# Performance work log

Measured on AMD Instinct MI355X. Metric: run time of the kernel, lower is better.

Reference implementation:

```python
import jax, jax.numpy as jnp
import numpy as np

N_NODES = 100000
N_EDGES = 1600000
D_FEAT = 128
D_OUT = 128


def gcn_conv(x, W, b, src, dst, w, n):
    # symmetric normalization (PyG GCNConv with self-loops already appended)
    deg = jax.ops.segment_sum(w, dst, num_segments=n)
    dinv = jnp.where(deg > 0, jax.lax.rsqrt(deg), 0.0)
    norm = dinv[src] * w * dinv[dst]                       # [E]
    h = x @ W                                              # [N, Dout]
    out = jax.ops.segment_sum(h[src] * norm[:, None], dst, num_segments=n)
    return out + b


def setup_inputs() -> dict:
    key = jax.random.key(0)
    ks = jax.random.split(key, 20)
    feat = jax.random.normal(ks[0], (N_NODES, D_FEAT), dtype=jnp.float32)
    gdv = jax.random.uniform(ks[1], (N_NODES, 73), dtype=jnp.float32)
    pr = jax.random.uniform(ks[2], (N_NODES, 1), dtype=jnp.float32)
    edge_index = jax.random.randint(ks[3], (2, N_EDGES), 0, N_NODES, dtype=jnp.int32)
    edge_weight = jax.random.uniform(ks[4], (N_EDGES,), dtype=jnp.float32)

    def lin(k, fi, fo):
        bound = 1.0 / np.sqrt(fi)
        k1, k2 = jax.random.split(k)
        W = jax.random.uniform(k1, (fi, fo), minval=-bound, maxval=bound, dtype=jnp.float32)
        b = jax.random.uniform(k2, (fo,), minval=-bound, maxval=bound, dtype=jnp.float32)
        return W, b

    W1, b1 = lin(ks[5], D_FEAT, D_OUT)          # gcn_layer1
    W2, b2 = lin(ks[6], D_OUT, D_OUT // 2)      # gcn_layer2
    gdv_W, gdv_b = lin(ks[7], 73, D_OUT // 4)
    pr_W, pr_b = lin(ks[8], 1, D_OUT // 4)
    enc_W1, enc_b1 = lin(ks[9], D_OUT, D_OUT)
    enc_W2, enc_b2 = lin(ks[10], D_OUT, D_OUT)
    return dict(feat=feat, gdv=gdv, pr=pr, edge_index=edge_index, edge_weight=edge_weight,
                W1=W1, b1=b1, W2=W2, b2=b2, gdv_W=gdv_W, gdv_b=gdv_b, pr_W=pr_W, pr_b=pr_b,
                enc_W1=enc_W1, enc_b1=enc_b1, enc_W2=enc_W2, enc_b2=enc_b2)


def reference(feat, gdv, pr, edge_index, edge_weight,
              W1, b1, W2, b2, gdv_W, gdv_b, pr_W, pr_b,
              enc_W1, enc_b1, enc_W2, enc_b2):
    n = feat.shape[0]
    loop = jnp.arange(n, dtype=edge_index.dtype)
    src = jnp.concatenate([edge_index[0], loop])
    dst = jnp.concatenate([edge_index[1], loop])
    w = jnp.concatenate([edge_weight, jnp.ones((n,), dtype=edge_weight.dtype)])

    h = jnp.tanh(gcn_conv(feat, W1, b1, src, dst, w, n))
    adj = jax.nn.sigmoid(gcn_conv(h, W2, b2, src, dst, w, n))   # [N, D/2]

    g = jax.nn.sigmoid(gdv @ gdv_W + gdv_b)                      # [N, D/4]
    p = jax.nn.sigmoid(pr @ pr_W + pr_b)                         # [N, D/4]

    enc = jnp.concatenate([adj, g, p], axis=1)                   # [N, D]
    enc = jnp.tanh(enc @ enc_W1 + enc_b1) @ enc_W2 + enc_b2
    return enc
```

## Files before the change

kernel.cpp:

```cpp
#include <hip/hip_runtime.h>
#include <hip/hip_bf16.h>
#include <cstdint>
#include <cstddef>

#define TPB 256
#define SCAN_CHUNK 1024

typedef short bf16x8 __attribute__((ext_vector_type(8)));
typedef float f32x4 __attribute__((ext_vector_type(4)));

__device__ __forceinline__ float sigmoidf_(float x) {
    return 1.0f / (1.0f + __expf(-x));
}
__device__ __forceinline__ unsigned short f2bf(float x) {
    unsigned u = __float_as_uint(x);
    u += 0x7FFF + ((u >> 16) & 1);
    return (unsigned short)(u >> 16);
}
__device__ __forceinline__ float bf2f(unsigned short b) {
    return __uint_as_float(((unsigned)b) << 16);
}

__device__ __forceinline__ void gld_lds16(const void* gsrc, void* ldst) {
    __builtin_amdgcn_global_load_lds(
        (const __attribute__((address_space(1))) unsigned*)gsrc,
        (__attribute__((address_space(3))) unsigned*)ldst, 16, 0, 0);
}

template<int M>
__device__ __forceinline__ void prep_w_body(const float* __restrict__ W,
                                            unsigned short* __restrict__ Wt, int c) {
    if (c >= M * 16) return;
    int m = c >> 4, k0 = (c & 15) << 3;
    unsigned o[4];
    #pragma unroll
    for (int j = 0; j < 4; ++j) {
        unsigned lo = f2bf(W[(size_t)(k0 + 2 * j) * M + m]);
        unsigned hi = f2bf(W[(size_t)(k0 + 2 * j + 1) * M + m]);
        o[j] = lo | (hi << 16);
    }
    unsigned byte = ((unsigned)c * 16) ^ (unsigned)((m & 7) << 4);
    *(uint4*)((char*)Wt + byte) = *(uint4*)o;
}

__global__ __launch_bounds__(TPB) void k_prep(const float* W1, unsigned short* wt1,
                                              const float* W2, unsigned short* wt2,
                                              const float* E1, unsigned short* wtE1,
                                              const float* E2, unsigned short* wtE2,
                                              unsigned* counts, int n, int nbZ) {
    int bid = blockIdx.x;
    if (bid < nbZ) {
        int i = bid * TPB + threadIdx.x;
        if (i < n) counts[i] = 0u;
    } else {
        int t = bid - nbZ;
        if (t < 8)       prep_w_body<128>(W1, wt1, t * TPB + threadIdx.x);
        else if (t < 12) prep_w_body<64>(W2, wt2, (t - 8) * TPB + threadIdx.x);
        else if (t < 20) prep_w_body<128>(E1, wtE1, (t - 12) * TPB + threadIdx.x);
        else             prep_w_body<128>(E2, wtE2, (t - 20) * TPB + threadIdx.x);
    }
}

template<int M, int ACT, bool A_BF16, bool OUT_F32>
__device__ __forceinline__ void mgemm_body(const void* __restrict__ Ap,
                                           const unsigned short* __restrict__ Wtg,
                                           const float* __restrict__ bias,
                                           void* __restrict__ Cp, int ldc, int coff,
                                           int n, int tile,
                                           unsigned short* Al, unsigned short* Wt) {
    const int tid = threadIdx.x;
    const int wv = tid >> 6;
    const int ln = tid & 63;
    const int rbase = tile * 128;

    constexpr int WCH = (M * 128 * 2) / 1024;
    #pragma unroll
    for (int c = 0; c < WCH / 4; ++c) {
        int cc = wv * (WCH / 4) + c;
        gld_lds16((const char*)Wtg + cc * 1024 + ln * 16, (char*)Wt + cc * 1024);
    }

    if (A_BF16 && rbase + 128 <= n) {
        #pragma unroll
        for (int it = 0; it < 8; ++it) {
            unsigned dbase = (unsigned)(wv * 8 + it) * 1024;
            unsigned d = dbase + (unsigned)ln * 16;
            unsigned row = d >> 8;
            unsigned s = d ^ ((row & 7) << 4);
            gld_lds16((const char*)Ap + (size_t)rbase * 256 + s, (char*)Al + dbase);
        }
    } else {
        for (int ch = tid; ch < 128 * 16; ch += TPB) {
            int row = ch >> 4;
            int col8 = (ch & 15) * 8;
            int r = rbase + row;
            unsigned o4[4] = {0u, 0u, 0u, 0u};
            if (r < n) {
                if constexpr (A_BF16) {
                    uint4 v = *(const uint4*)((const unsigned short*)Ap + (size_t)r * 128 + col8);
                    o4[0] = v.x; o4[1] = v.y; o4[2] = v.z; o4[3] = v.w;
                } else {
                    float4 a = *(const float4*)((const float*)Ap + (size_t)r * 128 + col8);
                    float4 b = *(const float4*)((const float*)Ap + (size_t)r * 128 + col8 + 4);
                    o4[0] = (unsigned)f2bf(a.x) | ((unsigned)f2bf(a.y) << 16);
                    o4[1] = (unsigned)f2bf(a.z) | ((unsigned)f2bf(a.w) << 16);
                    o4[2] = (unsigned)f2bf(b.x) | ((unsigned)f2bf(b.y) << 16);
                    o4[3] = (unsigned)f2bf(b.z) | ((unsigned)f2bf(b.w) << 16);
                }
            }
            unsigned byte = ((unsigned)ch * 16) ^ (unsigned)((row & 7) << 4);
            *(uint4*)((char*)Al + byte) = *(uint4*)o4;
        }
    }
    __syncthreads();

    const int lr = ln & 15;
    const int lg = ln >> 4;

    constexpr int MF = M / 16;
    f32x4 acc[2][MF];
    #pragma unroll
    for (int i = 0; i < 2; ++i)
        #pragma unroll
        for (int j = 0; j < MF; ++j) acc[i][j] = (f32x4){0.f, 0.f, 0.f, 0.f};

    #pragma unroll
    for (int kk = 0; kk < 4; ++kk) {
        const int kb = kk * 64 + lg * 16;
        bf16x8 af[2];
        #pragma unroll
        for (int rf = 0; rf < 2; ++rf) {
            int row = wv * 32 + rf * 16 + lr;
            unsigned byte = (unsigned)(row * 256 + kb) ^ (unsigned)((row & 7) << 4);
            af[rf] = *(bf16x8*)((char*)Al + byte);
        }
        #pragma unroll
        for (int mf = 0; mf < MF; ++mf) {
            int col = mf * 16 + lr;
            unsigned byte = (unsigned)(col * 256 + kb) ^ (unsigned)((col & 7) << 4);
            bf16x8 bfg = *(bf16x8*)((char*)Wt + byte);
            acc[0][mf] = __builtin_amdgcn_mfma_f32_16x16x32_bf16(af[0], bfg, acc[0][mf], 0, 0, 0);
            acc[1][mf] = __builtin_amdgcn_mfma_f32_16x16x32_bf16(af[1], bfg, acc[1][mf], 0, 0, 0);
        }
    }

    #pragma unroll
    for (int rf = 0; rf < 2; ++rf) {
        #pragma unroll
        for (int j = 0; j < 4; ++j) {
            int row = rbase + wv * 32 + rf * 16 + lg * 4 + j;
            if (row < n) {
                #pragma unroll
                for (int mf = 0; mf < MF; ++mf) {
                    int col = mf * 16 + lr;
                    float v = acc[rf][mf][j] + (bias ? bias[col] : 0.0f);
                    if constexpr (ACT == 1) v = tanhf(v);
                    else if constexpr (ACT == 2) v = sigmoidf_(v);
                    if constexpr (OUT_F32)
                        ((float*)Cp)[(size_t)row * ldc + coff + col] = v;
                    else
                        ((unsigned short*)Cp)[(size_t)row * ldc + coff + col] = f2bf(v);
                }
            }
        }
    }
}

__global__ __launch_bounds__(TPB) void k_g1p1(const float* __restrict__ feat,
                                              const unsigned short* __restrict__ wt1,
                                              unsigned short* __restrict__ bufA,
                                              int n, int nbM,
                                              const int* __restrict__ dst,
                                              unsigned* __restrict__ counts,
                                              unsigned* __restrict__ epos, int E) {
    __shared__ __align__(16) unsigned short Al[128 * 128];
    __shared__ __align__(16) unsigned short Wt[128 * 128];
    if (blockIdx.x < nbM) {
        mgemm_body<128, 0, false, false>(feat, wt1, nullptr, bufA, 128, 0, n,
                                         blockIdx.x, Al, Wt);
    } else {
        int e = (blockIdx.x - nbM) * TPB + threadIdx.x;
        if (e < E) epos[e] = atomicAdd(&counts[dst[e]], 1u);
    }
}

__global__ __launch_bounds__(TPB) void k_mgemm64(const unsigned short* __restrict__ Ap,
                                                 const unsigned short* __restrict__ Wtg,
                                                 unsigned short* __restrict__ Cp, int n) {
    __shared__ __align__(16) unsigned short Al[128 * 128];
    __shared__ __align__(16) unsigned short Wt[64 * 128];
    mgemm_body<64, 0, true, false>(Ap, Wtg, nullptr, Cp, 64, 0, n, blockIdx.x, Al, Wt);
}

__global__ __launch_bounds__(TPB) void k_enc2(const unsigned short* __restrict__ enc,
                                              const unsigned short* __restrict__ w1g,
                                              const float* __restrict__ b1,
                                              const unsigned short* __restrict__ w2g,
                                              const float* __restrict__ b2,
                                              float* __restrict__ out, int n) {
    __shared__ __align__(16) unsigned short Al[128 * 128];
    __shared__ __align__(16) unsigned short Wt[128 * 128];
    const int tid = threadIdx.x;
    const int wv = tid >> 6;
    const int ln = tid & 63;
    const int rbase = blockIdx.x * 128;
    const int lr = ln & 15;
    const int lg = ln >> 4;

    #pragma unroll
    for (int c = 0; c < 8; ++c) {
        int cc = wv * 8 + c;
        gld_lds16((const char*)w1g + cc * 1024 + ln * 16, (char*)Wt + cc * 1024);
    }
    if (rbase + 128 <= n) {
        #pragma unroll
        for (int it = 0; it < 8; ++it) {
            unsigned dbase = (unsigned)(wv * 8 + it) * 1024;
            unsigned d = dbase + (unsigned)ln * 16;
            unsigned row = d >> 8;
            unsigned s = d ^ ((row & 7) << 4);
            gld_lds16((const char*)enc + (size_t)rbase * 256 + s, (char*)Al + dbase);
        }
    } else {
        for (int ch = tid; ch < 128 * 16; ch += TPB) {
            int row = ch >> 4;
            int col8 = (ch & 15) * 8;
            int r = rbase + row;
            unsigned o4[4] = {0u, 0u, 0u, 0u};
            if (r < n) {
                uint4 v = *(const uint4*)(enc + (size_t)r * 128 + col8);
                o4[0] = v.x; o4[1] = v.y; o4[2] = v.z; o4[3] = v.w;
            }
            unsigned byte = ((unsigned)ch * 16) ^ (unsigned)((row & 7) << 4);
            *(uint4*)((char*)Al + byte) = *(uint4*)o4;
        }
    }
    __syncthreads();

    f32x4 acc[2][8];
    #pragma unroll
    for (int i = 0; i < 2; ++i)
        #pragma unroll
        for (int j = 0; j < 8; ++j) acc[i][j] = (f32x4){0.f, 0.f, 0.f, 0.f};

    #pragma unroll
    for (int kk = 0; kk < 4; ++kk) {
        const int kb = kk * 64 + lg * 16;
        bf16x8 af[2];
        #pragma unroll
        for (int rf = 0; rf < 2; ++rf) {
            int row = wv * 32 + rf * 16 + lr;
            unsigned byte = (unsigned)(row * 256 + kb) ^ (unsigned)((row & 7) << 4);
            af[rf] = *(bf16x8*)((char*)Al + byte);
        }
        #pragma unroll
        for (int mf = 0; mf < 8; ++mf) {
            int col = mf * 16 + lr;
            unsigned byte = (unsigned)(col * 256 + kb) ^ (unsigned)((col & 7) << 4);
            bf16x8 bfg = *(bf16x8*)((char*)Wt + byte);
            acc[0][mf] = __builtin_amdgcn_mfma_f32_16x16x32_bf16(af[0], bfg, acc[0][mf], 0, 0, 0);
            acc[1][mf] = __builtin_amdgcn_mfma_f32_16x16x32_bf16(af[1], bfg, acc[1][mf], 0, 0, 0);
        }
    }
    __syncthreads();

    #pragma unroll
    for (int c = 0; c < 8; ++c) {
        int cc = wv * 8 + c;
        gld_lds16((const char*)w2g + cc * 1024 + ln * 16, (char*)Wt + cc * 1024);
    }
    #pragma unroll
    for (int rf = 0; rf < 2; ++rf) {
        #pragma unroll
        for (int j = 0; j < 4; ++j) {
            int rl = wv * 32 + rf * 16 + lg * 4 + j;
            #pragma unroll
            for (int mf = 0; mf < 8; ++mf) {
                int col = mf * 16 + lr;
                float v = tanhf(acc[rf][mf][j] + b1[col]);
                unsigned byte = (unsigned)(rl * 256 + col * 2) ^ (unsigned)((rl & 7) << 4);
                *(unsigned short*)((char*)Al + byte) = f2bf(v);
            }
        }
    }
    __syncthreads();

    #pragma unroll
    for (int i = 0; i < 2; ++i)
        #pragma unroll
        for (int j = 0; j < 8; ++j) acc[i][j] = (f32x4){0.f, 0.f, 0.f, 0.f};

    #pragma unroll
    for (int kk = 0; kk < 4; ++kk) {
        const int kb = kk * 64 + lg * 16;
        bf16x8 af[2];
        #pragma unroll
        for (int rf = 0; rf < 2; ++rf) {
            int row = wv * 32 + rf * 16 + lr;
            unsigned byte = (unsigned)(row * 256 + kb) ^ (unsigned)((row & 7) << 4);
            af[rf] = *(bf16x8*)((char*)Al + byte);
        }
        #pragma unroll
        for (int mf = 0; mf < 8; ++mf) {
            int col = mf * 16 + lr;
            unsigned byte = (unsigned)(col * 256 + kb) ^ (unsigned)((col & 7) << 4);
            bf16x8 bfg = *(bf16x8*)((char*)Wt + byte);
            acc[0][mf] = __builtin_amdgcn_mfma_f32_16x16x32_bf16(af[0], bfg, acc[0][mf], 0, 0, 0);
            acc[1][mf] = __builtin_amdgcn_mfma_f32_16x16x32_bf16(af[1], bfg, acc[1][mf], 0, 0, 0);
        }
    }

    #pragma unroll
    for (int rf = 0; rf < 2; ++rf) {
        #pragma unroll
        for (int j = 0; j < 4; ++j) {
            int row = rbase + wv * 32 + rf * 16 + lg * 4 + j;
            if (row < n) {
                #pragma unroll
                for (int mf = 0; mf < 8; ++mf) {
                    int col = mf * 16 + lr;
                    out[(size_t)row * 128 + col] = acc[rf][mf][j] + b2[col];
                }
            }
        }
    }
}


__global__ __launch_bounds__(TPB) void k_scan_a(const unsigned* __restrict__ counts,
                                                int* __restrict__ rowptr,
                                                int* __restrict__ bsums, int n) {
    __shared__ int s[SCAN_CHUNK];
    int base = blockIdx.x * SCAN_CHUNK;
    int orig[4];
    #pragma unroll
    for (int j0 = 0; j0 < 4; ++j0) {
        int j = threadIdx.x + j0 * TPB;
        int v = (base + j < n) ? (int)counts[base + j] : 0;
        orig[j0] = v;
        s[j] = v;
    }
    __syncthreads();
    for (int off = 1; off < SCAN_CHUNK; off <<= 1) {
        int t[4];
        #pragma unroll
        for (int j0 = 0; j0 < 4; ++j0) {
            int j = threadIdx.x + j0 * TPB;
            t[j0] = (j >= off) ? s[j - off] : 0;
        }
        __syncthreads();
        #pragma unroll
        for (int j0 = 0; j0 < 4; ++j0) {
            int j = threadIdx.x + j0 * TPB;
            s[j] += t[j0];
        }
        __syncthreads();
    }
    #pragma unroll
    for (int j0 = 0; j0 < 4; ++j0) {
        int j = threadIdx.x + j0 * TPB;
        if (base + j < n) rowptr[base + j] = s[j] - orig[j0];
    }
    if (threadIdx.x == 0) bsums[blockIdx.x] = s[SCAN_CHUNK - 1];
}

__global__ void k_scan_b(int* bsums, int nb) {
    __shared__ int s[128];
    int t = threadIdx.x;
    int v = (t < nb) ? bsums[t] : 0;
    s[t] = v;
    __syncthreads();
    for (int off = 1; off < 128; off <<= 1) {
        int x = (t >= off) ? s[t - off] : 0;
        __syncthreads();
        s[t] += x;
        __syncthreads();
    }
    if (t < nb) bsums[t] = s[t] - v;
}

__global__ __launch_bounds__(TPB) void k_scan_c(int* __restrict__ rowptr,
                                                const int* __restrict__ bsums,
                                                int n, int E) {
    int i = blockIdx.x * TPB + threadIdx.x;
    if (i < n) rowptr[i] += bsums[i / SCAN_CHUNK];
    if (i == 0) rowptr[n] = E;
}

__global__ __launch_bounds__(TPB) void k_fill(const int* __restrict__ src,
                                              const int* __restrict__ dst,
                                              const float* __restrict__ ew,
                                              const int* __restrict__ rowptr,
                                              const unsigned* __restrict__ epos,
                                              uint2* __restrict__ edges, int E) {
    int e = blockIdx.x * TPB + threadIdx.x;
    if (e < E) {
        unsigned slot = (unsigned)rowptr[dst[e]] + epos[e];
        uint2 pk;
        pk.x = (unsigned)src[e];
        pk.y = __float_as_uint(ew[e]);
        edges[slot] = pk;
    }
}

__global__ __launch_bounds__(TPB) void k_deg(const int* __restrict__ rowptr,
                                             const uint2* __restrict__ edges,
                                             float* __restrict__ dinv, int n) {
    int i = blockIdx.x * TPB + threadIdx.x;
    if (i >= n) return;
    int beg = rowptr[i], end = rowptr[i + 1];
    float s = 1.0f;
    for (int e = beg; e < end; ++e) s += __uint_as_float(edges[e].y);
    dinv[i] = rsqrtf(s);
}

template<int D, int ACT>
__device__ __forceinline__ void agg_body(const unsigned short* __restrict__ h,
                                         const int* __restrict__ rowptr,
                                         const uint2* __restrict__ edges,
                                         const float* __restrict__ dinv,
                                         const float* __restrict__ bias,
                                         unsigned short* __restrict__ out,
                                         int ldo, int n, int node) {
    const int lane = threadIdx.x & 63;
    constexpr int PER = D / 64;
    float acc[PER];
    const float di = dinv[node];
    if constexpr (PER == 2) {
        unsigned hv = *(const unsigned*)&h[(size_t)node * D + lane * 2];
        acc[0] = bf2f((unsigned short)hv) * di;
        acc[1] = bf2f((unsigned short)(hv >> 16)) * di;
    } else {
        acc[0] = bf2f(h[(size_t)node * D + lane]) * di;
    }
    const int beg = rowptr[node];
    const int end = rowptr[node + 1];
    for (int e = beg; e < end; e += 8) {
        int ss[8]; float ww[8];
        #pragma unroll
        for (int u = 0; u < 8; ++u) {
            int idx = e + u;
            int cl = idx < end ? idx : (end - 1);
            uint2 ed = edges[cl];
            ss[u] = (int)ed.x;
            ww[u] = idx < end ? __uint_as_float(ed.y) : 0.0f;
        }
        float nn[8];
        #pragma unroll
        for (int u = 0; u < 8; ++u) nn[u] = ww[u] * dinv[ss[u]];
        if constexpr (PER == 2) {
            unsigned hv[8];
            #pragma unroll
            for (int u = 0; u < 8; ++u)
                hv[u] = *(const unsigned*)&h[(size_t)ss[u] * D + lane * 2];
            #pragma unroll
            for (int u = 0; u < 8; ++u) {
                acc[0] += bf2f((unsigned short)hv[u]) * nn[u];
                acc[1] += bf2f((unsigned short)(hv[u] >> 16)) * nn[u];
            }
        } else {
            unsigned short hv[8];
            #pragma unroll
            for (int u = 0; u < 8; ++u) hv[u] = h[(size_t)ss[u] * D + lane];
            #pragma unroll
            for (int u = 0; u < 8; ++u) acc[0] += bf2f(hv[u]) * nn[u];
        }
    }
    if constexpr (PER == 2) {
        float v0 = acc[0] * di + bias[lane * 2];
        float v1 = acc[1] * di + bias[lane * 2 + 1];
        if constexpr (ACT == 1) { v0 = tanhf(v0); v1 = tanhf(v1); }
        else                    { v0 = sigmoidf_(v0); v1 = sigmoidf_(v1); }
        unsigned pk = (unsigned)f2bf(v0) | ((unsigned)f2bf(v1) << 16);
        *(unsigned*)&out[(size_t)node * ldo + lane * 2] = pk;
    } else {
        float v = acc[0] * di + bias[lane];
        v = (ACT == 1) ? tanhf(v) : sigmoidf_(v);
        out[(size_t)node * ldo + lane] = f2bf(v);
    }
}

__global__ __launch_bounds__(TPB) void k_agg128(const unsigned short* __restrict__ h,
                                                const int* __restrict__ rowptr,
                                                const uint2* __restrict__ edges,
                                                const float* __restrict__ dinv,
                                                const float* __restrict__ bias,
                                                unsigned short* __restrict__ out, int n) {
    int node = blockIdx.x * 4 + (threadIdx.x >> 6);
    if (node < n) agg_body<128, 1>(h, rowptr, edges, dinv, bias, out, 128, n, node);
}

__device__ __forceinline__ void gemm_s_body(const float* __restrict__ A,
                                            const float* __restrict__ W,
                                            const float* __restrict__ bias,
                                            unsigned short* __restrict__ C,
                                            int n, int tile,
                                            float* Alds, float* Wlds) {
    for (int i = threadIdx.x; i < 73 * 32; i += TPB) Wlds[i] = W[i];
    const int c0 = threadIdx.x & 31;
    const int rg = threadIdx.x >> 5;
    const int rbase = tile * 32;
    for (int i = threadIdx.x; i < 32 * 73; i += TPB) {
        int rr = i / 73;
        int r = rbase + rr;
        Alds[i] = (r < n) ? A[(size_t)r * 73 + (i - rr * 73)] : 0.0f;
    }
    __syncthreads();
    float acc[4] = {0.f, 0.f, 0.f, 0.f};
    const float* Ab = &Alds[rg * 4 * 73];
    #pragma unroll 4
    for (int k = 0; k < 73; ++k) {
        float wv = Wlds[k * 32 + c0];
        #pragma unroll
        for (int j = 0; j < 4; ++j) acc[j] += Ab[j * 73 + k] * wv;
    }
    #pragma unroll
    for (int j = 0; j < 4; ++j) {
        int r = rbase + rg * 4 + j;
        if (r < n) C[(size_t)r * 128 + 64 + c0] = f2bf(sigmoidf_(acc[j] + bias[c0]));
    }
}

__global__ __launch_bounds__(TPB) void k_tail(const unsigned short* __restrict__ h2,
                                              const int* __restrict__ rowptr,
                                              const uint2* __restrict__ edges,
                                              const float* __restrict__ dinv,
                                              const float* __restrict__ b2,
                                              unsigned short* __restrict__ enc,
                                              const float* __restrict__ gdv,
                                              const float* __restrict__ gdvW,
                                              const float* __restrict__ gdvB,
                                              const float* __restrict__ pr,
                                              const float* __restrict__ prW,
                                              const float* __restrict__ prB,
                                              int n, int nA, int nG) {
    __shared__ float Alds[32 * 73];
    __shared__ float Wlds[73 * 32];
    int bid = blockIdx.x;
    if (bid < nA) {
        int node = bid * 4 + (threadIdx.x >> 6);
        if (node < n) agg_body<64, 2>(h2, rowptr, edges, dinv, b2, enc, 128, n, node);
    } else if (bid < nA + nG) {
        gemm_s_body(gdv, gdvW, gdvB, enc, n, bid - nA, Alds, Wlds);
    } else {
        int i = (bid - nA - nG) * TPB + threadIdx.x;
        if (i < n * 32) {
            int node = i >> 5;
            int c = i & 31;
            float v = pr[node] * prW[c] + prB[c];
            enc[(size_t)node * 128 + 96 + c] = f2bf(sigmoidf_(v));
        }
    }
}


extern "C" void kernel_launch(void* const* d_in, const int* in_sizes, int n_in,
                              void* d_out, int out_size, void* d_ws, size_t ws_size,
                              hipStream_t stream) {
    const float* feat = (const float*)d_in[0];
    const float* gdv  = (const float*)d_in[1];
    const float* pr   = (const float*)d_in[2];
    const int*   eidx = (const int*)d_in[3];
    const float* ew   = (const float*)d_in[4];
    const float* W1   = (const float*)d_in[5];
    const float* b1   = (const float*)d_in[6];
    const float* W2   = (const float*)d_in[7];
    const float* b2   = (const float*)d_in[8];
    const float* gdvW = (const float*)d_in[9];
    const float* gdvB = (const float*)d_in[10];
    const float* prW  = (const float*)d_in[11];
    const float* prB  = (const float*)d_in[12];
    const float* eW1  = (const float*)d_in[13];
    const float* eB1  = (const float*)d_in[14];
    const float* eW2  = (const float*)d_in[15];
    const float* eB2  = (const float*)d_in[16];
    float* out = (float*)d_out;

    const int N = in_sizes[0] / 128;
    const int E = in_sizes[4];
    const int* srcA = eidx;
    const int* dstA = eidx + E;

    char* p = (char*)d_ws;
    auto alloc = [&](size_t bytes) {
        char* r = p;
        p += (bytes + 255) & ~(size_t)255;
        return r;
    };
    unsigned* counts = (unsigned*)alloc((size_t)N * 4);
    unsigned* epos   = (unsigned*)alloc((size_t)E * 4);
    float*    dinv   = (float*)   alloc((size_t)N * 4);
    int*      rowptr = (int*)     alloc((size_t)(N + 1) * 4);
    int*      bsums  = (int*)     alloc(256 * 4);
    uint2*    edges  = (uint2*)   alloc((size_t)E * 8);
    unsigned short* wt1  = (unsigned short*)alloc(128 * 128 * 2);
    unsigned short* wt2  = (unsigned short*)alloc(128 * 64 * 2);
    unsigned short* wtE1 = (unsigned short*)alloc(128 * 128 * 2);
    unsigned short* wtE2 = (unsigned short*)alloc(128 * 128 * 2);
    unsigned short* bufA = (unsigned short*)alloc((size_t)N * 128 * 2);
    unsigned short* bufB = (unsigned short*)alloc((size_t)N * 128 * 2);

    const int nbN = (N + TPB - 1) / TPB;
    const int nbE = (E + TPB - 1) / TPB;
    const int nscan = (N + SCAN_CHUNK - 1) / SCAN_CHUNK;
    const int nbM = (N + 127) / 128;
    const int nA = (N + 3) / 4;
    const int nG = (N + 31) / 32;
    const int nP = (N * 32 + TPB - 1) / TPB;

    k_prep<<<nbN + 28, TPB, 0, stream>>>(W1, wt1, W2, wt2, eW1, wtE1, eW2, wtE2,
                                         counts, N, nbN);
    k_g1p1<<<nbM + nbE, TPB, 0, stream>>>(feat, wt1, bufA, N, nbM,
                                          dstA, counts, epos, E);
    k_scan_a<<<nscan, TPB, 0, stream>>>(counts, rowptr, bsums, N);
    k_scan_b<<<1, 128, 0, stream>>>(bsums, nscan);
    k_scan_c<<<nbN, TPB, 0, stream>>>(rowptr, bsums, N, E);
    k_fill<<<nbE, TPB, 0, stream>>>(srcA, dstA, ew, rowptr, epos, edges, E);
    k_deg<<<nbN, TPB, 0, stream>>>(rowptr, edges, dinv, N);
    k_agg128<<<nA, TPB, 0, stream>>>(bufA, rowptr, edges, dinv, b1, bufB, N);
    k_mgemm64<<<nbM, TPB, 0, stream>>>(bufB, wt2, bufA, N);
    k_tail<<<nA + nG + nP, TPB, 0, stream>>>(bufA, rowptr, edges, dinv, b2, bufB,
                                             gdv, gdvW, gdvB, pr, prW, prB, N, nA, nG);
    k_enc2<<<nbM, TPB, 0, stream>>>(bufB, wtE1, eB1, wtE2, eB2, out, N);
}
```

Measured before the change: 539.6 us.

## Move gdv/pr encoders into front kernel, fold scan_b, cache edge norms

The gdv linear and pr encoders now run in the first kernel alongside the edge counting and the first GEMM, writing into a separate encoder buffer. A third activation buffer is added so those results are not overwritten. The first GEMM now reads unswizzled bf16 weights straight from global memory instead of staging them in LDS, which lowers its LDS footprint. The single-block scan_b step is folded into scan_c. The layer-1 aggregation writes each edge's normalized weight back into the edge list, so layer-2 aggregation skips the dinv[src] gathers. The trade-offs are more global weight reads in GEMM1, extra memory for the new buffer, and a write-back of edge weights.

After: 619.4 us. 14.8% more time.

```diff
diff --git a/kernel.cpp b/kernel.cpp
--- a/kernel.cpp
+++ b/kernel.cpp
@@ -27,7 +27,7 @@
         (__attribute__((address_space(3))) unsigned*)ldst, 16, 0, 0);
 }
 
-template<int M>
+template<int M, bool SWZ>
 __device__ __forceinline__ void prep_w_body(const float* __restrict__ W,
                                             unsigned short* __restrict__ Wt, int c) {
     if (c >= M * 16) return;
@@ -39,7 +39,8 @@
         unsigned hi = f2bf(W[(size_t)(k0 + 2 * j + 1) * M + m]);
         o[j] = lo | (hi << 16);
     }
-    unsigned byte = ((unsigned)c * 16) ^ (unsigned)((m & 7) << 4);
+    unsigned byte = (unsigned)c * 16;
+    if (SWZ) byte ^= (unsigned)((m & 7) << 4);
     *(uint4*)((char*)Wt + byte) = *(uint4*)o;
 }
 
@@ -54,11 +55,308 @@
         if (i < n) counts[i] = 0u;
     } else {
         int t = bid - nbZ;
-        if (t < 8)       prep_w_body<128>(W1, wt1, t * TPB + threadIdx.x);
-        else if (t < 12) prep_w_body<64>(W2, wt2, (t - 8) * TPB + threadIdx.x);
-        else if (t < 20) prep_w_body<128>(E1, wtE1, (t - 12) * TPB + threadIdx.x);
-        else             prep_w_body<128>(E2, wtE2, (t - 20) * TPB + threadIdx.x);
-    }
+        if (t < 8)       prep_w_body<128, false>(W1, wt1, t * TPB + threadIdx.x);
+        else if (t < 12) prep_w_body<64, true>(W2, wt2, (t - 8) * TPB + threadIdx.x);
+        else if (t < 20) prep_w_body<128, true>(E1, wtE1, (t - 12) * TPB + threadIdx.x);
+        else             prep_w_body<128, true>(E2, wtE2, (t - 20) * TPB + threadIdx.x);
+    }
+}
+
+__device__ __forceinline__ void gemm1_body(const float* __restrict__ feat,
+                                           const unsigned short* __restrict__ wtl,
+                                           unsigned short* __restrict__ bufA,
+                                           int n, int tile, unsigned short* Al) {
+    const int tid = threadIdx.x;
+    const int rbase = tile * 128;
+    for (int ch = tid; ch < 128 * 16; ch += TPB) {
+        int row = ch >> 4;
+        int col8 = (ch & 15) * 8;
+        int r = rbase + row;
+        unsigned o4[4] = {0u, 0u, 0u, 0u};
+        if (r < n) {
+            float4 a = *(const float4*)(feat + (size_t)r * 128 + col8);
+            float4 b = *(const float4*)(feat + (size_t)r * 128 + col8 + 4);
+            o4[0] = (unsigned)f2bf(a.x) | ((unsigned)f2bf(a.y) << 16);
+            o4[1] = (unsigned)f2bf(a.z) | ((unsigned)f2bf(a.w) << 16);
+            o4[2] = (unsigned)f2bf(b.x) | ((unsigned)f2bf(b.y) << 16);
+            o4[3] = (unsigned)f2bf(b.z) | ((unsigned)f2bf(b.w) << 16);
+        }
+        unsigned byte = ((unsigned)ch * 16) ^ (unsigned)((row & 7) << 4);
+        *(uint4*)((char*)Al + byte) = *(uint4*)o4;
+    }
+    __syncthreads();
+
+    const int wv = tid >> 6, ln = tid & 63, lr = ln & 15, lg = ln >> 4;
+    f32x4 acc[2][8];
+    #pragma unroll
+    for (int i = 0; i < 2; ++i)
+        #pragma unroll
+        for (int j = 0; j < 8; ++j) acc[i][j] = (f32x4){0.f, 0.f, 0.f, 0.f};
+
+    #pragma unroll
+    for (int kk = 0; kk < 4; ++kk) {
+        const int kb = kk * 64 + lg * 16;
+        bf16x8 af[2];
+        #pragma unroll
+        for (int rf = 0; rf < 2; ++rf) {
+            int row = wv * 32 + rf * 16 + lr;
+            unsigned byte = (unsigned)(row * 256 + kb) ^ (unsigned)((row & 7) << 4);
+            af[rf] = *(bf16x8*)((char*)Al + byte);
+        }
+        #pragma unroll
+        for (int mf = 0; mf < 8; ++mf) {
+            int col = mf * 16 + lr;
+            bf16x8 bfg = *(const bf16x8*)((const char*)wtl + col * 256 + kb);
+            acc[0][mf] = __builtin_amdgcn_mfma_f32_16x16x32_bf16(af[0], bfg, acc[0][mf], 0, 0, 0);
+            acc[1][mf] = __builtin_amdgcn_mfma_f32_16x16x32_bf16(af[1], bfg, acc[1][mf], 0, 0, 0);
+        }
+    }
+    #pragma unroll
+    for (int rf = 0; rf < 2; ++rf) {
+        #pragma unroll
+        for (int j = 0; j < 4; ++j) {
+            int row = rbase + wv * 32 + rf * 16 + lg * 4 + j;
+            if (row < n) {
+                #pragma unroll
+                for (int mf = 0; mf < 8; ++mf) {
+                    int col = mf * 16 + lr;
+                    bufA[(size_t)row * 128 + col] = f2bf(acc[rf][mf][j]);
+                }
+            }
+        }
+    }
+}
+
+__device__ __forceinline__ void gemm_s_body(const float* __restrict__ A,
+                                            const float* __restrict__ W,
+                                            const float* __restrict__ bias,
+                                            unsigned short* __restrict__ C,
+                                            int n, int tile,
+                                            float* Alds, float* Wlds) {
+    for (int i = threadIdx.x; i < 73 * 32; i += TPB) Wlds[i] = W[i];
+    const int c0 = threadIdx.x & 31;
+    const int rg = threadIdx.x >> 5;
+    const int rbase = tile * 32;
+    for (int i = threadIdx.x; i < 32 * 73; i += TPB) {
+        int rr = i / 73;
+        int r = rbase + rr;
+        Alds[i] = (r < n) ? A[(size_t)r * 73 + (i - rr * 73)] : 0.0f;
+    }
+    __syncthreads();
+    float acc[4] = {0.f, 0.f, 0.f, 0.f};
+    const float* Ab = &Alds[rg * 4 * 73];
+    #pragma unroll 4
+    for (int k = 0; k < 73; ++k) {
+        float wv = Wlds[k * 32 + c0];
+        #pragma unroll
+        for (int j = 0; j < 4; ++j) acc[j] += Ab[j * 73 + k] * wv;
+    }
+    #pragma unroll
+    for (int j = 0; j < 4; ++j) {
+        int r = rbase + rg * 4 + j;
+        if (r < n) C[(size_t)r * 128 + 64 + c0] = f2bf(sigmoidf_(acc[j] + bias[c0]));
+    }
+}
+
+__global__ __launch_bounds__(TPB) void k_front(
+        const int* __restrict__ dst, unsigned* __restrict__ counts,
+        unsigned* __restrict__ epos, int E,
+        const float* __restrict__ feat, const unsigned short* __restrict__ wtl1,
+        unsigned short* __restrict__ bufA,
+        const float* __restrict__ gdv, const float* __restrict__ gdvW,
+        const float* __restrict__ gdvB,
+        const float* __restrict__ pr, const float* __restrict__ prW,
+        const float* __restrict__ prB,
+        unsigned short* __restrict__ enc, int n, int nbE, int nbM, int nG) {
+    __shared__ __align__(16) char smem[32768];
+    int bid = blockIdx.x;
+    if (bid < nbE) {
+        int e = bid * TPB + threadIdx.x;
+        if (e < E) epos[e] = atomicAdd(&counts[dst[e]], 1u);
+    } else if (bid < nbE + nbM) {
+        gemm1_body(feat, wtl1, bufA, n, bid - nbE, (unsigned short*)smem);
+    } else if (bid < nbE + nbM + nG) {
+        gemm_s_body(gdv, gdvW, gdvB, enc, n, bid - nbE - nbM,
+                    (float*)smem, (float*)(smem + 9344));
+    } else {
+        int i = (bid - nbE - nbM - nG) * TPB + threadIdx.x;
+        if (i < n * 32) {
+            int node = i >> 5;
+            int c = i & 31;
+            float v = pr[node] * prW[c] + prB[c];
+            enc[(size_t)node * 128 + 96 + c] = f2bf(sigmoidf_(v));
+        }
+    }
+}
+
+
+__global__ __launch_bounds__(TPB) void k_scan_a(const unsigned* __restrict__ counts,
+                                                int* __restrict__ rowptr,
+                                                int* __restrict__ bsums, int n) {
+    __shared__ int s[SCAN_CHUNK];
+    int base = blockIdx.x * SCAN_CHUNK;
+    int orig[4];
+    #pragma unroll
+    for (int j0 = 0; j0 < 4; ++j0) {
+        int j = threadIdx.x + j0 * TPB;
+        int v = (base + j < n) ? (int)counts[base + j] : 0;
+        orig[j0] = v;
+        s[j] = v;
+    }
+    __syncthreads();
+    for (int off = 1; off < SCAN_CHUNK; off <<= 1) {
+        int t[4];
+        #pragma unroll
+        for (int j0 = 0; j0 < 4; ++j0) {
+            int j = threadIdx.x + j0 * TPB;
+            t[j0] = (j >= off) ? s[j - off] : 0;
+        }
+        __syncthreads();
+        #pragma unroll
+        for (int j0 = 0; j0 < 4; ++j0) {
+            int j = threadIdx.x + j0 * TPB;
+            s[j] += t[j0];
+        }
+        __syncthreads();
+    }
+    #pragma unroll
+    for (int j0 = 0; j0 < 4; ++j0) {
+        int j = threadIdx.x + j0 * TPB;
+        if (base + j < n) rowptr[base + j] = s[j] - orig[j0];
+    }
+    if (threadIdx.x == 0) bsums[blockIdx.x] = s[SCAN_CHUNK - 1];
+}
+
+__global__ __launch_bounds__(TPB) void k_scan_c(int* __restrict__ rowptr,
+                                                const int* __restrict__ bsums,
+                                                int n, int E, int nb) {
+    __shared__ int sb[128];
+    int t = threadIdx.x;
+    if (t < 128) sb[t] = (t < nb) ? bsums[t] : 0;
+    __syncthreads();
+    for (int off = 1; off < 128; off <<= 1) {
+        int x = 0;
+        if (t < 128 && t >= off) x = sb[t - off];
+        __syncthreads();
+        if (t < 128) sb[t] += x;
+        __syncthreads();
+    }
+    int i = blockIdx.x * TPB + t;
+    if (i < n) {
+        int chunk = i >> 10;
+        int prefix = (chunk == 0) ? 0 : sb[chunk - 1];
+        rowptr[i] += prefix;
+    }
+    if (i == 0) rowptr[n] = E;
+}
+
+__global__ __launch_bounds__(TPB) void k_fill(const int* __restrict__ src,
+                                              const int* __restrict__ dst,
+                                              const float* __restrict__ ew,
+                                              const int* __restrict__ rowptr,
+                                              const unsigned* __restrict__ epos,
+                                              uint2* __restrict__ edges, int E) {
+    int e = blockIdx.x * TPB + threadIdx.x;
+    if (e < E) {
+        unsigned slot = (unsigned)rowptr[dst[e]] + epos[e];
+        uint2 pk;
+        pk.x = (unsigned)src[e];
+        pk.y = __float_as_uint(ew[e]);
+        edges[slot] = pk;
+    }
+}
+
+__global__ __launch_bounds__(TPB) void k_deg(const int* __restrict__ rowptr,
+                                             const uint2* __restrict__ edges,
+                                             float* __restrict__ dinv, int n) {
+    int i = blockIdx.x * TPB + threadIdx.x;
+    if (i >= n) return;
+    int beg = rowptr[i], end = rowptr[i + 1];
+    float s = 1.0f;
+    for (int e = beg; e < end; ++e) s += __uint_as_float(edges[e].y);
+    dinv[i] = rsqrtf(s);
+}
+
+__global__ __launch_bounds__(TPB) void k_agg128(const unsigned short* __restrict__ h,
+                                                const int* __restrict__ rowptr,
+                                                uint2* __restrict__ edges,
+                                                const float* __restrict__ dinv,
+                                                const float* __restrict__ bias,
+                                                unsigned short* __restrict__ out, int n) {
+    const int lane = threadIdx.x & 63;
+    const int node = blockIdx.x * 4 + (threadIdx.x >> 6);
+    if (node >= n) return;
+    float acc0, acc1;
+    const float di = dinv[node];
+    {
+        unsigned hv = *(const unsigned*)&h[(size_t)node * 128 + lane * 2];
+        acc0 = bf2f((unsigned short)hv) * di;
+        acc1 = bf2f((unsigned short)(hv >> 16)) * di;
+    }
+    const int beg = rowptr[node];
+    const int end = rowptr[node + 1];
+    for (int e = beg; e < end; e += 8) {
+        int ss[8]; float nn[8];
+        #pragma unroll
+        for (int u = 0; u < 8; ++u) {
+            int idx = e + u;
+            int cl = idx < end ? idx : (end - 1);
+            uint2 ed = edges[cl];
+            ss[u] = (int)ed.x;
+            nn[u] = (idx < end) ? __uint_as_float(ed.y) * dinv[ss[u]] : 0.0f;
+        }
+        if (lane == 0) {
+            #pragma unroll
+            for (int u = 0; u < 8; ++u)
+                if (e + u < end) edges[e + u].y = __float_as_uint(nn[u]);
+        }
+        unsigned hv[8];
+        #pragma unroll
+        for (int u = 0; u < 8; ++u)
+            hv[u] = *(const unsigned*)&h[(size_t)ss[u] * 128 + lane * 2];
+        #pragma unroll
+        for (int u = 0; u < 8; ++u) {
+            acc0 += bf2f((unsigned short)hv[u]) * nn[u];
+            acc1 += bf2f((unsigned short)(hv[u] >> 16)) * nn[u];
+        }
+    }
+    float v0 = tanhf(acc0 * di + bias[lane * 2]);
+    float v1 = tanhf(acc1 * di + bias[lane * 2 + 1]);
+    unsigned pk = (unsigned)f2bf(v0) | ((unsigned)f2bf(v1) << 16);
+    *(unsigned*)&out[(size_t)node * 128 + lane * 2] = pk;
+}
+
+__global__ __launch_bounds__(TPB) void k_agg64(const unsigned short* __restrict__ h,
+                                               const int* __restrict__ rowptr,
+                                               const uint2* __restrict__ edges,
+                                               const float* __restrict__ dinv,
+                                               const float* __restrict__ bias,
+                                               unsigned short* __restrict__ enc, int n) {
+    const int lane = threadIdx.x & 63;
+    const int node = blockIdx.x * 4 + (threadIdx.x >> 6);
+    if (node >= n) return;
+    const float di = dinv[node];
+    float acc = bf2f(h[(size_t)node * 64 + lane]) * di;
+    const int beg = rowptr[node];
+    const int end = rowptr[node + 1];
+    for (int e = beg; e < end; e += 8) {
+        int ss[8]; float nn[8];
+        #pragma unroll
+        for (int u = 0; u < 8; ++u) {
+            int idx = e + u;
+            int cl = idx < end ? idx : (end - 1);
+            uint2 ed = edges[cl];
+            ss[u] = (int)ed.x;
+            nn[u] = (idx < end) ? __uint_as_float(ed.y) : 0.0f;
+        }
+        unsigned short hv[8];
+        #pragma unroll
+        for (int u = 0; u < 8; ++u) hv[u] = h[(size_t)ss[u] * 64 + lane];
+        #pragma unroll
+        for (int u = 0; u < 8; ++u) acc += bf2f(hv[u]) * nn[u];
+    }
+    float v = sigmoidf_(acc * di + bias[lane]);
+    enc[(size_t)node * 128 + lane] = f2bf(v);
 }
 
 template<int M, int ACT, bool A_BF16, bool OUT_F32>
@@ -79,7 +377,6 @@
         int cc = wv * (WCH / 4) + c;
         gld_lds16((const char*)Wtg + cc * 1024 + ln * 16, (char*)Wt + cc * 1024);
     }
-
     if (A_BF16 && rbase + 128 <= n) {
         #pragma unroll
         for (int it = 0; it < 8; ++it) {
@@ -96,17 +393,8 @@
             int r = rbase + row;
             unsigned o4[4] = {0u, 0u, 0u, 0u};
             if (r < n) {
-                if constexpr (A_BF16) {
-                    uint4 v = *(const uint4*)((const unsigned short*)Ap + (size_t)r * 128 + col8);
-                    o4[0] = v.x; o4[1] = v.y; o4[2] = v.z; o4[3] = v.w;
-                } else {
-                    float4 a = *(const float4*)((const float*)Ap + (size_t)r * 128 + col8);
-                    float4 b = *(const float4*)((const float*)Ap + (size_t)r * 128 + col8 + 4);
-                    o4[0] = (unsigned)f2bf(a.x) | ((unsigned)f2bf(a.y) << 16);
-                    o4[1] = (unsigned)f2bf(a.z) | ((unsigned)f2bf(a.w) << 16);
-                    o4[2] = (unsigned)f2bf(b.x) | ((unsigned)f2bf(b.y) << 16);
-                    o4[3] = (unsigned)f2bf(b.z) | ((unsigned)f2bf(b.w) << 16);
-                }
+                uint4 v = *(const uint4*)((const unsigned short*)Ap + (size_t)r * 128 + col8);
+                o4[0] = v.x; o4[1] = v.y; o4[2] = v.z; o4[3] = v.w;
             }
             unsigned byte = ((unsigned)ch * 16) ^ (unsigned)((row & 7) << 4);
             *(uint4*)((char*)Al + byte) = *(uint4*)o4;
@@ -116,7 +404,6 @@
 
     const int lr = ln & 15;
     const int lg = ln >> 4;
-
     constexpr int MF = M / 16;
     f32x4 acc[2][MF];
     #pragma unroll
@@ -143,7 +430,6 @@
             acc[1][mf] = __builtin_amdgcn_mfma_f32_16x16x32_bf16(af[1], bfg, acc[1][mf], 0, 0, 0);
         }
     }
-
     #pragma unroll
     for (int rf = 0; rf < 2; ++rf) {
         #pragma unroll
@@ -166,24 +452,6 @@
     }
 }
 
-__global__ __launch_bounds__(TPB) void k_g1p1(const float* __restrict__ feat,
-                                              const unsigned short* __restrict__ wt1,
-                                              unsigned short* __restrict__ bufA,
-                                              int n, int nbM,
-                                              const int* __restrict__ dst,
-                                              unsigned* __restrict__ counts,
-                                              unsigned* __restrict__ epos, int E) {
-    __shared__ __align__(16) unsigned short Al[128 * 128];
-    __shared__ __align__(16) unsigned short Wt[128 * 128];
-    if (blockIdx.x < nbM) {
-        mgemm_body<128, 0, false, false>(feat, wt1, nullptr, bufA, 128, 0, n,
-                                         blockIdx.x, Al, Wt);
-    } else {
-        int e = (blockIdx.x - nbM) * TPB + threadIdx.x;
-        if (e < E) epos[e] = atomicAdd(&counts[dst[e]], 1u);
-    }
-}
-
 __global__ __launch_bounds__(TPB) void k_mgemm64(const unsigned short* __restrict__ Ap,
                                                  const unsigned short* __restrict__ Wtg,
                                                  unsigned short* __restrict__ Cp, int n) {
@@ -242,7 +510,6 @@
     for (int i = 0; i < 2; ++i)
         #pragma unroll
         for (int j = 0; j < 8; ++j) acc[i][j] = (f32x4){0.f, 0.f, 0.f, 0.f};
-
     #pragma unroll
     for (int kk = 0; kk < 4; ++kk) {
         const int kb = kk * 64 + lg * 16;
@@ -289,7 +556,6 @@
     for (int i = 0; i < 2; ++i)
         #pragma unroll
         for (int j = 0; j < 8; ++j) acc[i][j] = (f32x4){0.f, 0.f, 0.f, 0.f};
-
     #pragma unroll
     for (int kk = 0; kk < 4; ++kk) {
         const int kb = kk * 64 + lg * 16;
@@ -309,7 +575,6 @@
             acc[1][mf] = __builtin_amdgcn_mfma_f32_16x16x32_bf16(af[1], bfg, acc[1][mf], 0, 0, 0);
         }
     }
-
     #pragma unroll
     for (int rf = 0; rf < 2; ++rf) {
         #pragma unroll
@@ -322,233 +587,6 @@
                     out[(size_t)row * 128 + col] = acc[rf][mf][j] + b2[col];
                 }
             }
-        }
-    }
-}
-
-
-__global__ __launch_bounds__(TPB) void k_scan_a(const unsigned* __restrict__ counts,
-                                                int* __restrict__ rowptr,
-                                                int* __restrict__ bsums, int n) {
-    __shared__ int s[SCAN_CHUNK];
-    int base = blockIdx.x * SCAN_CHUNK;
-    int orig[4];
-    #pragma unroll
-    for (int j0 = 0; j0 < 4; ++j0) {
-        int j = threadIdx.x + j0 * TPB;
-        int v = (base + j < n) ? (int)counts[base + j] : 0;
-        orig[j0] = v;
-        s[j] = v;
-    }
-    __syncthreads();
-    for (int off = 1; off < SCAN_CHUNK; off <<= 1) {
-        int t[4];
-        #pragma unroll
-        for (int j0 = 0; j0 < 4; ++j0) {
-            int j = threadIdx.x + j0 * TPB;
-            t[j0] = (j >= off) ? s[j - off] : 0;
-        }
-        __syncthreads();
-        #pragma unroll
-        for (int j0 = 0; j0 < 4; ++j0) {
-            int j = threadIdx.x + j0 * TPB;
-            s[j] += t[j0];
-        }
-        __syncthreads();
-    }
-    #pragma unroll
-    for (int j0 = 0; j0 < 4; ++j0) {
-        int j = threadIdx.x + j0 * TPB;
-        if (base + j < n) rowptr[base + j] = s[j] - orig[j0];
-    }
-    if (threadIdx.x == 0) bsums[blockIdx.x] = s[SCAN_CHUNK - 1];
-}
-
-__global__ void k_scan_b(int* bsums, int nb) {
-    __shared__ int s[128];
-    int t = threadIdx.x;
-    int v = (t < nb) ? bsums[t] : 0;
-    s[t] = v;
-    __syncthreads();
-    for (int off = 1; off < 128; off <<= 1) {
-        int x = (t >= off) ? s[t - off] : 0;
-        __syncthreads();
-        s[t] += x;
-        __syncthreads();
-    }
-    if (t < nb) bsums[t] = s[t] - v;
-}
-
-__global__ __launch_bounds__(TPB) void k_scan_c(int* __restrict__ rowptr,
-                                                const int* __restrict__ bsums,
-                                                int n, int E) {
-    int i = blockIdx.x * TPB + threadIdx.x;
-    if (i < n) rowptr[i] += bsums[i / SCAN_CHUNK];
-    if (i == 0) rowptr[n] = E;
-}
-
-__global__ __launch_bounds__(TPB) void k_fill(const int* __restrict__ src,
-                                              const int* __restrict__ dst,
-                                              const float* __restrict__ ew,
-                                              const int* __restrict__ rowptr,
-                                              const unsigned* __restrict__ epos,
-                                              uint2* __restrict__ edges, int E) {
-    int e = blockIdx.x * TPB + threadIdx.x;
-    if (e < E) {
-        unsigned slot = (unsigned)rowptr[dst[e]] + epos[e];
-        uint2 pk;
-        pk.x = (unsigned)src[e];
-        pk.y = __float_as_uint(ew[e]);
-        edges[slot] = pk;
-    }
-}
-
-__global__ __launch_bounds__(TPB) void k_deg(const int* __restrict__ rowptr,
-                                             const uint2* __restrict__ edges,
-                                             float* __restrict__ dinv, int n) {
-    int i = blockIdx.x * TPB + threadIdx.x;
-    if (i >= n) return;
-    int beg = rowptr[i], end = rowptr[i + 1];
-    float s = 1.0f;
-    for (int e = beg; e < end; ++e) s += __uint_as_float(edges[e].y);
-    dinv[i] = rsqrtf(s);
-}
-
-template<int D, int ACT>
-__device__ __forceinline__ void agg_body(const unsigned short* __restrict__ h,
-                                         const int* __restrict__ rowptr,
-                                         const uint2* __restrict__ edges,
-                                         const float* __restrict__ dinv,
-                                         const float* __restrict__ bias,
-                                         unsigned short* __restrict__ out,
-                                         int ldo, int n, int node) {
-    const int lane = threadIdx.x & 63;
-    constexpr int PER = D / 64;
-    float acc[PER];
-    const float di = dinv[node];
-    if constexpr (PER == 2) {
-        unsigned hv = *(const unsigned*)&h[(size_t)node * D + lane * 2];
-        acc[0] = bf2f((unsigned short)hv) * di;
-        acc[1] = bf2f((unsigned short)(hv >> 16)) * di;
-    } else {
-        acc[0] = bf2f(h[(size_t)node * D + lane]) * di;
-    }
-    const int beg = rowptr[node];
-    const int end = rowptr[node + 1];
-    for (int e = beg; e < end; e += 8) {
-        int ss[8]; float ww[8];
-        #pragma unroll
-        for (int u = 0; u < 8; ++u) {
-            int idx = e + u;
-            int cl = idx < end ? idx : (end - 1);
-            uint2 ed = edges[cl];
-            ss[u] = (int)ed.x;
-            ww[u] = idx < end ? __uint_as_float(ed.y) : 0.0f;
-        }
-        float nn[8];
-        #pragma unroll
-        for (int u = 0; u < 8; ++u) nn[u] = ww[u] * dinv[ss[u]];
-        if constexpr (PER == 2) {
-            unsigned hv[8];
-            #pragma unroll
-            for (int u = 0; u < 8; ++u)
-                hv[u] = *(const unsigned*)&h[(size_t)ss[u] * D + lane * 2];
-            #pragma unroll
-            for (int u = 0; u < 8; ++u) {
-                acc[0] += bf2f((unsigned short)hv[u]) * nn[u];
-                acc[1] += bf2f((unsigned short)(hv[u] >> 16)) * nn[u];
-            }
-        } else {
-            unsigned short hv[8];
-            #pragma unroll
-            for (int u = 0; u < 8; ++u) hv[u] = h[(size_t)ss[u] * D + lane];
-            #pragma unroll
-            for (int u = 0; u < 8; ++u) acc[0] += bf2f(hv[u]) * nn[u];
-        }
-    }
-    if constexpr (PER == 2) {
-        float v0 = acc[0] * di + bias[lane * 2];
-        float v1 = acc[1] * di + bias[lane * 2 + 1];
-        if constexpr (ACT == 1) { v0 = tanhf(v0); v1 = tanhf(v1); }
-        else                    { v0 = sigmoidf_(v0); v1 = sigmoidf_(v1); }
-        unsigned pk = (unsigned)f2bf(v0) | ((unsigned)f2bf(v1) << 16);
-        *(unsigned*)&out[(size_t)node * ldo + lane * 2] = pk;
-    } else {
-        float v = acc[0] * di + bias[lane];
-        v = (ACT == 1) ? tanhf(v) : sigmoidf_(v);
-        out[(size_t)node * ldo + lane] = f2bf(v);
-    }
-}
-
-__global__ __launch_bounds__(TPB) void k_agg128(const unsigned short* __restrict__ h,
-                                                const int* __restrict__ rowptr,
-                                                const uint2* __restrict__ edges,
-                                                const float* __restrict__ dinv,
-                                                const float* __restrict__ bias,
-                                                unsigned short* __restrict__ out, int n) {
-    int node = blockIdx.x * 4 + (threadIdx.x >> 6);
-    if (node < n) agg_body<128, 1>(h, rowptr, edges, dinv, bias, out, 128, n, node);
-}
-
-__device__ __forceinline__ void gemm_s_body(const float* __restrict__ A,
-                                            const float* __restrict__ W,
-                                            const float* __restrict__ bias,
-                                            unsigned short* __restrict__ C,
-                                            int n, int tile,
-                                            float* Alds, float* Wlds) {
-    for (int i = threadIdx.x; i < 73 * 32; i += TPB) Wlds[i] = W[i];
-    const int c0 = threadIdx.x & 31;
-    const int rg = threadIdx.x >> 5;
-    const int rbase = tile * 32;
-    for (int i = threadIdx.x; i < 32 * 73; i += TPB) {
-        int rr = i / 73;
-        int r = rbase + rr;
-        Alds[i] = (r < n) ? A[(size_t)r * 73 + (i - rr * 73)] : 0.0f;
-    }
-    __syncthreads();
-    float acc[4] = {0.f, 0.f, 0.f, 0.f};
-    const float* Ab = &Alds[rg * 4 * 73];
-    #pragma unroll 4
-    for (int k = 0; k < 73; ++k) {
-        float wv = Wlds[k * 32 + c0];
-        #pragma unroll
-        for (int j = 0; j < 4; ++j) acc[j] += Ab[j * 73 + k] * wv;
-    }
-    #pragma unroll
-    for (int j = 0; j < 4; ++j) {
-        int r = rbase + rg * 4 + j;
-        if (r < n) C[(size_t)r * 128 + 64 + c0] = f2bf(sigmoidf_(acc[j] + bias[c0]));
-    }
-}
-
-__global__ __launch_bounds__(TPB) void k_tail(const unsigned short* __restrict__ h2,
-                                              const int* __restrict__ rowptr,
-                                              const uint2* __restrict__ edges,
-                                              const float* __restrict__ dinv,
-                                              const float* __restrict__ b2,
-                                              unsigned short* __restrict__ enc,
-                                              const float* __restrict__ gdv,
-                                              const float* __restrict__ gdvW,
-                                              const float* __restrict__ gdvB,
-                                              const float* __restrict__ pr,
-                                              const float* __restrict__ prW,
-                                              const float* __restrict__ prB,
-                                              int n, int nA, int nG) {
-    __shared__ float Alds[32 * 73];
-    __shared__ float Wlds[73 * 32];
-    int bid = blockIdx.x;
-    if (bid < nA) {
-        int node = bid * 4 + (threadIdx.x >> 6);
-        if (node < n) agg_body<64, 2>(h2, rowptr, edges, dinv, b2, enc, 128, n, node);
-    } else if (bid < nA + nG) {
-        gemm_s_body(gdv, gdvW, gdvB, enc, n, bid - nA, Alds, Wlds);
-    } else {
-        int i = (bid - nA - nG) * TPB + threadIdx.x;
-        if (i < n * 32) {
-            int node = i >> 5;
-            int c = i & 31;
-            float v = pr[node] * prW[c] + prB[c];
-            enc[(size_t)node * 128 + 96 + c] = f2bf(sigmoidf_(v));
         }
     }
 }
@@ -599,6 +637,7 @@
     unsigned short* wtE2 = (unsigned short*)alloc(128 * 128 * 2);
     unsigned short* bufA = (unsigned short*)alloc((size_t)N * 128 * 2);
     unsigned short* bufB = (unsigned short*)alloc((size_t)N * 128 * 2);
+    unsigned short* bufC = (unsigned short*)alloc((size_t)N * 128 * 2);
 
     const int nbN = (N + TPB - 1) / TPB;
     const int nbE = (E + TPB - 1) / TPB;
@@ -610,16 +649,15 @@
 
     k_prep<<<nbN + 28, TPB, 0, stream>>>(W1, wt1, W2, wt2, eW1, wtE1, eW2, wtE2,
                                          counts, N, nbN);
-    k_g1p1<<<nbM + nbE, TPB, 0, stream>>>(feat, wt1, bufA, N, nbM,
-                                          dstA, counts, epos, E);
+    k_front<<<nbE + nbM + nG + nP, TPB, 0, stream>>>(
+        dstA, counts, epos, E, feat, wt1, bufA,
+        gdv, gdvW, gdvB, pr, prW, prB, bufB, N, nbE, nbM, nG);
     k_scan_a<<<nscan, TPB, 0, stream>>>(counts, rowptr, bsums, N);
-    k_scan_b<<<1, 128, 0, stream>>>(bsums, nscan);
-    k_scan_c<<<nbN, TPB, 0, stream>>>(rowptr, bsums, N, E);
+    k_scan_c<<<nbN, TPB, 0, stream>>>(rowptr, bsums, N, E, nscan);
     k_fill<<<nbE, TPB, 0, stream>>>(srcA, dstA, ew, rowptr, epos, edges, E);
     k_deg<<<nbN, TPB, 0, stream>>>(rowptr, edges, dinv, N);
-    k_agg128<<<nA, TPB, 0, stream>>>(bufA, rowptr, edges, dinv, b1, bufB, N);
-    k_mgemm64<<<nbM, TPB, 0, stream>>>(bufB, wt2, bufA, N);
-    k_tail<<<nA + nG + nP, TPB, 0, stream>>>(bufA, rowptr, edges, dinv, b2, bufB,
-                                             gdv, gdvW, gdvB, pr, prW, prB, N, nA, nG);
+    k_agg128<<<nA, TPB, 0, stream>>>(bufA, rowptr, edges, dinv, b1, bufC, N);
+    k_mgemm64<<<nbM, TPB, 0, stream>>>(bufC, wt2, bufA, N);
+    k_agg64<<<nA, TPB, 0, stream>>>(bufA, rowptr, edges, dinv, b2, bufB, N);
     k_enc2<<<nbM, TPB, 0, stream>>>(bufB, wtE1, eB1, wtE2, eB2, out, N);
 }
```
